# Performance work log

Hardware: AMD Instinct MI355X
Metric: run time of the kernel (lower is better)

## Reference

```python
import jax, jax.numpy as jnp
import numpy as np

N = 2708
IN_C = 1433
OUT_C = 64


def setup_inputs() -> dict:
    key = jax.random.key(0)
    k1, k2, k3, k4, k5, k6, k7 = jax.random.split(key, 7)
    X = jax.random.normal(k1, (N, IN_C), dtype=jnp.float32)
    A = jax.random.randint(k2, (N, N), 0, 2, dtype=jnp.int32)  # dense binary adjacency mask
    # Graph Fourier basis: orthonormal-ish random matrix (QR of gaussian)
    U = jnp.linalg.qr(jax.random.normal(k3, (N, N), dtype=jnp.float32))[0]
    s = 1.0 / np.sqrt(IN_C)
    W_K = jax.random.normal(k4, (OUT_C, IN_C), dtype=jnp.float32) * s
    W_Q = jax.random.normal(k5, (OUT_C, IN_C), dtype=jnp.float32) * s
    W_V = jax.random.normal(k6, (OUT_C, IN_C), dtype=jnp.float32) * s
    lmbd = jax.random.uniform(k7, (N, 1), dtype=jnp.float32)
    return {"X": X, "A": A, "U": U, "W_K": W_K, "W_Q": W_Q, "W_V": W_V, "lmbd": lmbd}


def reference(X, A, U, W_K, W_Q, W_V, lmbd):
    # Linear projections (torch nn.Linear: x @ W.T)
    K = X @ W_K.T  # [N, d]
    Q = X @ W_Q.T  # [N, d]
    V = X @ W_V.T  # [N, d]
    d_k = K.shape[-1]
    E = (Q @ K.T) / d_k  # [N, N]
    # spectral filtering: igft(lmbd * gft(E)) = U @ (lmbd * (U^T @ E))
    E = jnp.abs(U @ (lmbd * (U.T @ E)))
    # masked softmax over neighbors; dropout p=0 in eval mode (no-op)
    E_masked = jnp.where(A == 0, -jnp.inf, E)
    alpha = jax.nn.softmax(E_masked, axis=-1)
    H = alpha @ V  # [N, d]
    return H
```

## Files before the change

kernel.cpp:

```cpp
#include <hip/hip_runtime.h>

#define NV 2708
#define INC 1433
#define XCOLS 1472
#define UDIM 2752
#define PSTR 2728
#define BSTR 2752
#define SLAB ((size_t)(2752*64))
#define MWPR 88
#define NSP 4
#define NSU 11

typedef __attribute__((ext_vector_type(8))) short bf16x8;
typedef __attribute__((ext_vector_type(4))) float f32x4;
typedef __attribute__((ext_vector_type(4))) unsigned short u16x4;

__device__ __forceinline__ unsigned short f2bf(float f){
  union { float f; unsigned int i; } v; v.f = f;
  return (unsigned short)((v.i + 0x7fffu + ((v.i >> 16) & 1u)) >> 16);
}

__device__ __forceinline__ void conv_row(const float* __restrict__ src,
                                         unsigned short* __restrict__ dst, int tid){
  const int sh = ((unsigned int)((size_t)src >> 2)) & 1;
  if (tid == 0){ int ce = sh ? 0 : (INC - 1); dst[ce] = f2bf(src[ce]); }
  const float2* s2 = (const float2*)(src + sh);
  for (int c2 = tid; c2 < (INC - 1)/2; c2 += 256){
    float2 v = s2[c2];
    int c = sh + c2*2;
    dst[c]     = f2bf(v.x);
    dst[c + 1] = f2bf(v.y);
  }
  for (int c = INC + tid; c < XCOLS; c += 256) dst[c] = 0;
}

__global__ __launch_bounds__(256) void convert_all(
    const float* __restrict__ X, const float* __restrict__ WK,
    const float* __restrict__ WQ, const float* __restrict__ WV,
    const float* __restrict__ U, const int* __restrict__ A,
    unsigned short* __restrict__ Xbf, unsigned short* __restrict__ Wbf,
    unsigned short* __restrict__ Ubf, unsigned short* __restrict__ UTbf,
    unsigned int* __restrict__ Abits)
{
  __shared__ __align__(16) float tpose[64][68];
  const int bx = blockIdx.x;
  const int tid = threadIdx.x;
  if (bx < 2752){
    const int row = bx;
    unsigned short* dst = Xbf + (size_t)row*XCOLS;
    if (row < NV){
      conv_row(X + (size_t)row*INC, dst, tid);
    } else {
      u16x4 zz = {0,0,0,0};
      for (int c4 = tid; c4 < XCOLS/4; c4 += 256) *(u16x4*)(dst + c4*4) = zz;
    }
  } else if (bx < 2944){
    const int row = bx - 2752;
    const float* s = (row < 64) ? WK : (row < 128) ? WQ : WV;
    conv_row(s + (size_t)(row & 63)*INC, Wbf + (size_t)row*XCOLS, tid);
  } else if (bx < 5652){
    const int i = bx - 2944;
    const int lane = tid & 63, wave = tid >> 6;
    const int* arow = A + (size_t)i*NV;
    unsigned int* drow = Abits + (size_t)i*MWPR;
    for (int g = wave; g < 11; g += 4){
      int base = g*256 + lane*4;
      int4 v = make_int4(0,0,0,0);
      if (base < NV) v = *(const int4*)(arow + base);
      unsigned long long m0 = __ballot(v.x != 0);
      unsigned long long m1 = __ballot(v.y != 0);
      unsigned long long m2 = __ballot(v.z != 0);
      unsigned long long m3 = __ballot(v.w != 0);
      if (lane < 8){
        unsigned long long mm = (lane < 2) ? m0 : (lane < 4) ? m1 : (lane < 6) ? m2 : m3;
        drow[g*8 + lane] = (lane & 1) ? (unsigned int)(mm >> 32) : (unsigned int)mm;
      }
    }
  } else {
    const int t = bx - 5652;
    const int tx = t % 43, ty = t / 43;
    const int r0 = ty*64, c0 = tx*64;
    #pragma unroll
    for (int j = 0; j < 4; j++){
      int row = j*16 + (tid >> 4);
      int c4  = (tid & 15)*4;
      float4 v = make_float4(0.f,0.f,0.f,0.f);
      if (r0 + row < NV && c0 + c4 < NV)
        v = *(const float4*)(U + (size_t)(r0+row)*NV + c0 + c4);
      *(float4*)&tpose[row][c4] = v;
      u16x4 h = { f2bf(v.x), f2bf(v.y), f2bf(v.z), f2bf(v.w) };
      *(u16x4*)(Ubf + (size_t)(r0+row)*UDIM + c0 + c4) = h;
    }
    __syncthreads();
    const int i = tid >> 2;
    #pragma unroll
    for (int j = 0; j < 4; j++){
      int kk = ((tid & 3) + j*4)*4;
      u16x4 h = { f2bf(tpose[kk+0][i]), f2bf(tpose[kk+1][i]),
                  f2bf(tpose[kk+2][i]), f2bf(tpose[kk+3][i]) };
      *(u16x4*)(UTbf + (size_t)(c0+i)*UDIM + r0 + kk) = h;
    }
  }
}

__global__ __launch_bounds__(256) void proj(
    const unsigned short* __restrict__ Xbf, const unsigned short* __restrict__ Wbf,
    float* __restrict__ part)
{
  __shared__ __align__(16) unsigned short At[32*72];
  __shared__ __align__(16) unsigned short Bt[64*72];
  const int tid = threadIdx.x;
  const int lane = tid & 63, wave = tid >> 6, quad = lane >> 4, lr = lane & 15;
  const int m0 = blockIdx.x * 32;
  const int s  = blockIdx.y, z = blockIdx.z;
  const int kbeg = s * 384, kend = min(kbeg + 384, XCOLS);
  const int wm = (wave & 1) * 16, wn = (wave >> 1) * 32;
  const unsigned short* Wz = Wbf + (size_t)z*64*XCOLS;
  const int arow = tid >> 3, aseg = tid & 7;
  const int brow = tid >> 2, bseg = tid & 3;
  f32x4 acc[2] = {};

  for (int k0 = kbeg; k0 < kend; k0 += 64){
    *(bf16x8*)&At[arow*72 + aseg*8] =
        *(const bf16x8*)(Xbf + (size_t)(m0+arow)*XCOLS + k0 + aseg*8);
    {
      const unsigned short* b = Wz + (size_t)brow*XCOLS + k0 + bseg*16;
      *(bf16x8*)&Bt[brow*72 + bseg*16]     = *(const bf16x8*)(b);
      *(bf16x8*)&Bt[brow*72 + bseg*16 + 8] = *(const bf16x8*)(b + 8);
    }
    __syncthreads();
    #pragma unroll
    for (int ks = 0; ks < 2; ks++){
      bf16x8 af = *(const bf16x8*)&At[(wm + lr)*72 + ks*32 + quad*8];
      bf16x8 bv[2];
      #pragma unroll
      for (int t = 0; t < 2; t++)
        bv[t] = *(const bf16x8*)&Bt[(wn + t*16 + lr)*72 + ks*32 + quad*8];
      #pragma unroll
      for (int t = 0; t < 2; t++)
        acc[t] = __builtin_amdgcn_mfma_f32_16x16x32_bf16(af, bv[t], acc[t], 0, 0, 0);
    }
    __syncthreads();
  }
  float* dst = part + (size_t)(z*NSP + s) * SLAB;
  #pragma unroll
  for (int t = 0; t < 2; t++)
    #pragma unroll
    for (int e = 0; e < 4; e++)
      dst[(size_t)(m0 + wm + quad*4 + e)*64 + wn + t*16 + lr] = acc[t][e];
}

__global__ __launch_bounds__(256) void reduce_proj(
    const float* __restrict__ part, unsigned short* __restrict__ K16f,
    unsigned short* __restrict__ QT16, unsigned short* __restrict__ VTf)
{
  int idx = blockIdx.x*256 + threadIdx.x;
  int z = blockIdx.y;
  int m = idx >> 6, c = idx & 63;
  const float* base = part + (size_t)z*NSP*SLAB + idx;
  float v = 0.f;
  #pragma unroll
  for (int s = 0; s < NSP; s++) v += base[s*SLAB];
  unsigned short h = (m < NV) ? f2bf(v) : (unsigned short)0;
  if (z == 0){
    if (m < 2720) K16f[((m>>4)*2 + (c>>5))*512 + (m&15)*32 + (c&31)] = h;
  } else if (z == 1){
    QT16[(size_t)c*BSTR + m] = h;
  } else {
    if (m < 2720) VTf[(m>>5)*2048 + c*32 + (m&31)] = h;
  }
}

__global__ __launch_bounds__(256) void gemmU(
    const unsigned short* __restrict__ Arow, const unsigned short* __restrict__ Bcm,
    float* __restrict__ part)
{
  __shared__ __align__(16) unsigned short At[32*72];
  __shared__ __align__(16) unsigned short Bt[64*72];
  const int tid = threadIdx.x;
  const int lane = tid & 63, wave = tid >> 6, quad = lane >> 4, lr = lane & 15;
  const int m0 = blockIdx.x * 32;
  const int s  = blockIdx.y;
  const int kbeg = s * 256, kend = min(kbeg + 256, UDIM);
  const int wm = (wave & 1) * 16, wn = (wave >> 1) * 32;
  const int arow = tid >> 3, aseg = tid & 7;
  const int bc = tid >> 2, bseg = tid & 3;
  f32x4 acc[2] = {};

  for (int k0 = kbeg; k0 < kend; k0 += 64){
    *(bf16x8*)&At[arow*72 + aseg*8] =
        *(const bf16x8*)(Arow + (size_t)(m0+arow)*UDIM + k0 + aseg*8);
    {
      const unsigned short* b = Bcm + (size_t)bc*BSTR + k0 + bseg*16;
      *(bf16x8*)&Bt[bc*72 + bseg*16]     = *(const bf16x8*)(b);
      *(bf16x8*)&Bt[bc*72 + bseg*16 + 8] = *(const bf16x8*)(b + 8);
    }
    __syncthreads();
    #pragma unroll
    for (int ks = 0; ks < 2; ks++){
      bf16x8 af = *(const bf16x8*)&At[(wm + lr)*72 + ks*32 + quad*8];
      bf16x8 bv[2];
      #pragma unroll
      for (int t = 0; t < 2; t++)
        bv[t] = *(const bf16x8*)&Bt[(wn + t*16 + lr)*72 + ks*32 + quad*8];
      #pragma unroll
      for (int t = 0; t < 2; t++)
        acc[t] = __builtin_amdgcn_mfma_f32_16x16x32_bf16(af, bv[t], acc[t], 0, 0, 0);
    }
    __syncthreads();
  }
  float* dst = part + (size_t)s * SLAB;
  #pragma unroll
  for (int t = 0; t < 2; t++)
    #pragma unroll
    for (int e = 0; e < 4; e++)
      dst[(size_t)(m0 + wm + quad*4 + e)*64 + wn + t*16 + lr] = acc[t][e];
}

__global__ __launch_bounds__(256) void reduce_g(
    const float* __restrict__ part, const float* __restrict__ lm,
    unsigned short* __restrict__ G2T)
{
  int idx = blockIdx.x*256 + threadIdx.x;
  int m = idx >> 6, c = idx & 63;
  const float* base = part + idx;
  float v = 0.f;
  #pragma unroll
  for (int s = 0; s < NSU; s++) v += base[s*SLAB];
  unsigned short h = 0;
  if (m < NV) h = f2bf(v * lm[m] * (1.0f/64.0f));
  G2T[(size_t)c*BSTR + m] = h;
}

__global__ __launch_bounds__(512) void fused_attn(
    const float* __restrict__ partF, const unsigned short* __restrict__ K16f,
    const unsigned int* __restrict__ Abits, const unsigned short* __restrict__ VTf,
    float* __restrict__ Hout)
{
  __shared__ __align__(16) unsigned short pbuf[16*PSTR];
  __shared__ __align__(16) unsigned short fbuf[16*64];
  __shared__ unsigned int mrow[16*MWPR];
  __shared__ float swave[8][16];
  __shared__ float rinv[16];
  __shared__ __align__(16) float obuf[4][256];
  const int tid  = threadIdx.x;
  const int lane = tid & 63, wave = tid >> 6;
  const int quad = lane >> 4, lr = lane & 15;
  const int i0 = blockIdx.x * 16;

  #pragma unroll
  for (int h = 0; h < 2; h++){
    int idx = h*512 + tid;
    const float* base = partF + (size_t)(i0 + (idx >> 6))*64 + (idx & 63);
    float v = 0.f;
    #pragma unroll
    for (int s = 0; s < NSU; s++) v += base[s*SLAB];
    fbuf[idx] = f2bf(v);
  }
  for (int idx = tid; idx < 16*MWPR; idx += 512){
    int r = idx / MWPR;
    unsigned int v = 0;
    if (i0 + r < NV) v = Abits[(size_t)(i0 + r)*MWPR + (idx - r*MWPR)];
    mrow[idx] = v;
  }
  __syncthreads();

  const bf16x8 af0 = *(const bf16x8*)&fbuf[lr*64 + quad*8];
  const bf16x8 af1 = *(const bf16x8*)&fbuf[lr*64 + 32 + quad*8];
  float psum[4] = {0.f, 0.f, 0.f, 0.f};
  {
    int t = wave;
    const unsigned short* kb = K16f + t*1024 + lr*32 + quad*8;
    bf16x8 b0 = *(const bf16x8*)(kb);
    bf16x8 b1 = *(const bf16x8*)(kb + 512);
    while (t < 170){
      int tn = t + 8;
      bf16x8 n0 = b0, n1 = b1;
      if (tn < 170){
        const unsigned short* nb = K16f + tn*1024 + lr*32 + quad*8;
        n0 = *(const bf16x8*)(nb);
        n1 = *(const bf16x8*)(nb + 512);
      }
      f32x4 sv0 = {}, sv1 = {};
      sv0 = __builtin_amdgcn_mfma_f32_16x16x32_bf16(af0, b0, sv0, 0, 0, 0);
      sv1 = __builtin_amdgcn_mfma_f32_16x16x32_bf16(af1, b1, sv1, 0, 0, 0);
      f32x4 sv = sv0 + sv1;
      {
        int col = t*16 + lr;
        int ss = col & 255, ll = ss >> 2;
        int wsh = (col >> 8)*8 + (ss & 3)*2 + (ll >> 5);
        int bit = ll & 31;
        #pragma unroll
        for (int e = 0; e < 4; e++){
          int r = quad*4 + e;
          float p = 0.f;
          if ((mrow[r*MWPR + wsh] >> bit) & 1u) p = __expf(fabsf(sv[e]));
          psum[e] += p;
          pbuf[r*PSTR + col] = f2bf(p);
        }
      }
      b0 = n0; b1 = n1; t = tn;
    }
  }
  #pragma unroll
  for (int e = 0; e < 4; e++){
    float v = psum[e];
    #pragma unroll
    for (int o = 1; o <= 8; o <<= 1) v += __shfl_xor(v, o, 64);
    if (lr == 0) swave[wave][quad*4 + e] = v;
  }
  __syncthreads();
  if (tid < 16){
    float s = 0.f;
    #pragma unroll
    for (int w = 0; w < 8; w++) s += swave[w][tid];
    rinv[tid] = (s > 0.f) ? (1.f/s) : 0.f;
  }
  __syncthreads();

  const int c0 = (wave & 3) * 16;
  const int ktbeg = (wave >> 2) ? 43 : 0;
  const int ktend = (wave >> 2) ? 85 : 43;
  f32x4 acc = {};
  {
    bf16x8 bv = *(const bf16x8*)&VTf[ktbeg*2048 + (c0 + lr)*32 + quad*8];
    for (int kt = ktbeg; kt < ktend; kt++){
      bf16x8 bn = bv;
      if (kt + 1 < ktend) bn = *(const bf16x8*)&VTf[(kt+1)*2048 + (c0 + lr)*32 + quad*8];
      bf16x8 af = *(const bf16x8*)&pbuf[lr*PSTR + kt*32 + quad*8];
      acc = __builtin_amdgcn_mfma_f32_16x16x32_bf16(af, bv, acc, 0, 0, 0);
      bv = bn;
    }
  }
  if (wave >= 4) *(f32x4*)&obuf[wave & 3][lane*4] = acc;
  __syncthreads();
  if (wave < 4){
    f32x4 o = *(const f32x4*)&obuf[wave][lane*4];
    acc += o;
    #pragma unroll
    for (int e = 0; e < 4; e++){
      int r = quad*4 + e;
      int i = i0 + r;
      if (i < NV) Hout[(size_t)i*64 + c0 + lr] = acc[e] * rinv[r];
    }
  }
}

extern "C" void kernel_launch(void* const* d_in, const int* in_sizes, int n_in,
                              void* d_out, int out_size, void* d_ws, size_t ws_size,
                              hipStream_t stream){
  (void)in_sizes; (void)n_in; (void)out_size; (void)ws_size;
  const float* X  = (const float*)d_in[0];
  const int*   A  = (const int*)d_in[1];
  const float* U  = (const float*)d_in[2];
  const float* WK = (const float*)d_in[3];
  const float* WQ = (const float*)d_in[4];
  const float* WV = (const float*)d_in[5];
  const float* lm = (const float*)d_in[6];

  char* ws = (char*)d_ws;
  size_t off = 0;
  auto alloc = [&](size_t bytes){ size_t o = off; off = (off + bytes + 255) & ~(size_t)255; return o; };
  float*          part = (float*)(ws + alloc(12*SLAB*4));
  unsigned short* Ubf  = (unsigned short*)(ws + alloc((size_t)UDIM*UDIM*2));
  unsigned short* UTbf = (unsigned short*)(ws + alloc((size_t)UDIM*UDIM*2));
  unsigned short* Xbf  = (unsigned short*)(ws + alloc((size_t)UDIM*XCOLS*2));
  unsigned short* Wbf  = (unsigned short*)(ws + alloc((size_t)192*XCOLS*2));
  unsigned short* K16f = (unsigned short*)(ws + alloc((size_t)170*1024*2));
  unsigned short* QT16 = (unsigned short*)(ws + alloc((size_t)64*BSTR*2));
  unsigned short* G2T  = (unsigned short*)(ws + alloc((size_t)64*BSTR*2));
  unsigned short* VTf  = (unsigned short*)(ws + alloc((size_t)85*2048*2));
  unsigned int*   Abits= (unsigned int*)(ws + alloc((size_t)NV*MWPR*4));

  convert_all<<<dim3(7501), 256, 0, stream>>>(X, WK, WQ, WV, U, A,
                                              Xbf, Wbf, Ubf, UTbf, Abits);
  proj<<<dim3(86, NSP, 3), 256, 0, stream>>>(Xbf, Wbf, part);
  reduce_proj<<<dim3(688, 3), 256, 0, stream>>>(part, K16f, QT16, VTf);
  gemmU<<<dim3(86, NSU), 256, 0, stream>>>(UTbf, QT16, part);
  reduce_g<<<dim3(688), 256, 0, stream>>>(part, lm, G2T);
  gemmU<<<dim3(86, NSU), 256, 0, stream>>>(Ubf, G2T, part);
  fused_attn<<<dim3(170), 512, 0, stream>>>(part, K16f, Abits, VTf, (float*)d_out);
}
```

Before: 176.5 us.

## Overlap U conversion and adjacency bit-packing with projection GEMM blocks

Moves the U bf16 conversion/transposition and the adjacency bitmask packing out of the convert kernel and into extra blocks of the projection kernel, so this memory-bound work runs alongside the projection MFMA blocks. The Q projection is no longer split along K: a single block per row tile computes the full reduction and writes the transposed bf16 QT directly, which removes Q from the partial-sum buffer and from the reduce pass. The intent is to cut serial dependency and shorten the convert kernel. In exchange, the projection grid gets much larger, with many early-exit blocks, and Q now runs as a long serial K loop across only a few blocks.

After: 179.9 us. Within noise of the previous version (+1.9%).

```diff
diff --git a/kernel.cpp b/kernel.cpp
--- a/kernel.cpp
+++ b/kernel.cpp
@@ -37,12 +37,8 @@
 __global__ __launch_bounds__(256) void convert_all(
     const float* __restrict__ X, const float* __restrict__ WK,
     const float* __restrict__ WQ, const float* __restrict__ WV,
-    const float* __restrict__ U, const int* __restrict__ A,
-    unsigned short* __restrict__ Xbf, unsigned short* __restrict__ Wbf,
-    unsigned short* __restrict__ Ubf, unsigned short* __restrict__ UTbf,
-    unsigned int* __restrict__ Abits)
-{
-  __shared__ __align__(16) float tpose[64][68];
+    unsigned short* __restrict__ Xbf, unsigned short* __restrict__ Wbf)
+{
   const int bx = blockIdx.x;
   const int tid = threadIdx.x;
   if (bx < 2752){
@@ -54,66 +50,86 @@
       u16x4 zz = {0,0,0,0};
       for (int c4 = tid; c4 < XCOLS/4; c4 += 256) *(u16x4*)(dst + c4*4) = zz;
     }
-  } else if (bx < 2944){
+  } else {
     const int row = bx - 2752;
     const float* s = (row < 64) ? WK : (row < 128) ? WQ : WV;
     conv_row(s + (size_t)(row & 63)*INC, Wbf + (size_t)row*XCOLS, tid);
-  } else if (bx < 5652){
-    const int i = bx - 2944;
-    const int lane = tid & 63, wave = tid >> 6;
-    const int* arow = A + (size_t)i*NV;
-    unsigned int* drow = Abits + (size_t)i*MWPR;
-    for (int g = wave; g < 11; g += 4){
-      int base = g*256 + lane*4;
-      int4 v = make_int4(0,0,0,0);
-      if (base < NV) v = *(const int4*)(arow + base);
-      unsigned long long m0 = __ballot(v.x != 0);
-      unsigned long long m1 = __ballot(v.y != 0);
-      unsigned long long m2 = __ballot(v.z != 0);
-      unsigned long long m3 = __ballot(v.w != 0);
-      if (lane < 8){
-        unsigned long long mm = (lane < 2) ? m0 : (lane < 4) ? m1 : (lane < 6) ? m2 : m3;
-        drow[g*8 + lane] = (lane & 1) ? (unsigned int)(mm >> 32) : (unsigned int)mm;
-      }
-    }
-  } else {
-    const int t = bx - 5652;
-    const int tx = t % 43, ty = t / 43;
-    const int r0 = ty*64, c0 = tx*64;
-    #pragma unroll
-    for (int j = 0; j < 4; j++){
-      int row = j*16 + (tid >> 4);
-      int c4  = (tid & 15)*4;
-      float4 v = make_float4(0.f,0.f,0.f,0.f);
-      if (r0 + row < NV && c0 + c4 < NV)
-        v = *(const float4*)(U + (size_t)(r0+row)*NV + c0 + c4);
-      *(float4*)&tpose[row][c4] = v;
-      u16x4 h = { f2bf(v.x), f2bf(v.y), f2bf(v.z), f2bf(v.w) };
-      *(u16x4*)(Ubf + (size_t)(r0+row)*UDIM + c0 + c4) = h;
-    }
-    __syncthreads();
-    const int i = tid >> 2;
-    #pragma unroll
-    for (int j = 0; j < 4; j++){
-      int kk = ((tid & 3) + j*4)*4;
-      u16x4 h = { f2bf(tpose[kk+0][i]), f2bf(tpose[kk+1][i]),
-                  f2bf(tpose[kk+2][i]), f2bf(tpose[kk+3][i]) };
-      *(u16x4*)(UTbf + (size_t)(c0+i)*UDIM + r0 + kk) = h;
-    }
   }
 }
 
 __global__ __launch_bounds__(256) void proj(
     const unsigned short* __restrict__ Xbf, const unsigned short* __restrict__ Wbf,
-    float* __restrict__ part)
-{
-  __shared__ __align__(16) unsigned short At[32*72];
-  __shared__ __align__(16) unsigned short Bt[64*72];
+    const float* __restrict__ U, const int* __restrict__ A,
+    float* __restrict__ part, unsigned short* __restrict__ QT16,
+    unsigned short* __restrict__ Ubf, unsigned short* __restrict__ UTbf,
+    unsigned int* __restrict__ Abits)
+{
+  __shared__ __align__(16) char smem[17408];
   const int tid = threadIdx.x;
+  const int bx = blockIdx.x;
+  const int s = blockIdx.y, z = blockIdx.z;
+
+  if (bx >= 86){
+    const int slot = s*3 + z;
+    if (bx < 312){
+      const int i = (bx - 86)*12 + slot;
+      if (i < NV){
+        const int lane = tid & 63, wave = tid >> 6;
+        const int* arow = A + (size_t)i*NV;
+        unsigned int* drow = Abits + (size_t)i*MWPR;
+        for (int g = wave; g < 11; g += 4){
+          int base = g*256 + lane*4;
+          int4 v = make_int4(0,0,0,0);
+          if (base < NV) v = *(const int4*)(arow + base);
+          unsigned long long m0 = __ballot(v.x != 0);
+          unsigned long long m1 = __ballot(v.y != 0);
+          unsigned long long m2 = __ballot(v.z != 0);
+          unsigned long long m3 = __ballot(v.w != 0);
+          if (lane < 8){
+            unsigned long long mm = (lane < 2) ? m0 : (lane < 4) ? m1 : (lane < 6) ? m2 : m3;
+            drow[g*8 + lane] = (lane & 1) ? (unsigned int)(mm >> 32) : (unsigned int)mm;
+          }
+        }
+      }
+    } else {
+      const int t = (bx - 312)*12 + slot;
+      if (t < 1849){
+        float* tpose = (float*)smem;
+        const int tx = t % 43, ty = t / 43;
+        const int r0 = ty*64, c0 = tx*64;
+        #pragma unroll
+        for (int j = 0; j < 4; j++){
+          int row = j*16 + (tid >> 4);
+          int c4  = (tid & 15)*4;
+          float4 v = make_float4(0.f,0.f,0.f,0.f);
+          if (r0 + row < NV && c0 + c4 < NV)
+            v = *(const float4*)(U + (size_t)(r0+row)*NV + c0 + c4);
+          *(float4*)&tpose[row*68 + c4] = v;
+          u16x4 h = { f2bf(v.x), f2bf(v.y), f2bf(v.z), f2bf(v.w) };
+          *(u16x4*)(Ubf + (size_t)(r0+row)*UDIM + c0 + c4) = h;
+        }
+        __syncthreads();
+        const int i = tid >> 2;
+        #pragma unroll
+        for (int j = 0; j < 4; j++){
+          int kk = ((tid & 3) + j*4)*4;
+          u16x4 h = { f2bf(tpose[(kk+0)*68 + i]), f2bf(tpose[(kk+1)*68 + i]),
+                      f2bf(tpose[(kk+2)*68 + i]), f2bf(tpose[(kk+3)*68 + i]) };
+          *(u16x4*)(UTbf + (size_t)(c0+i)*UDIM + r0 + kk) = h;
+        }
+      }
+    }
+    return;
+  }
+
+  const bool isQ = (z == 1);
+  if (isQ && s) return;
+  unsigned short* At = (unsigned short*)smem;
+  unsigned short* Bt = (unsigned short*)(smem + 4608);
   const int lane = tid & 63, wave = tid >> 6, quad = lane >> 4, lr = lane & 15;
-  const int m0 = blockIdx.x * 32;
-  const int s  = blockIdx.y, z = blockIdx.z;
-  const int kbeg = s * 384, kend = min(kbeg + 384, XCOLS);
+  const int m0 = bx * 32;
+  const int kbeg = isQ ? 0 : s * 384;
+  const int kend = isQ ? XCOLS : min(kbeg + 384, XCOLS);
   const int wm = (wave & 1) * 16, wn = (wave >> 1) * 32;
   const unsigned short* Wz = Wbf + (size_t)z*64*XCOLS;
   const int arow = tid >> 3, aseg = tid & 7;
@@ -142,32 +158,40 @@
     }
     __syncthreads();
   }
-  float* dst = part + (size_t)(z*NSP + s) * SLAB;
-  #pragma unroll
-  for (int t = 0; t < 2; t++)
-    #pragma unroll
-    for (int e = 0; e < 4; e++)
-      dst[(size_t)(m0 + wm + quad*4 + e)*64 + wn + t*16 + lr] = acc[t][e];
+  if (isQ){
+    #pragma unroll
+    for (int t = 0; t < 2; t++)
+      #pragma unroll
+      for (int e = 0; e < 4; e++){
+        int m = m0 + wm + quad*4 + e;
+        int c = wn + t*16 + lr;
+        QT16[(size_t)c*BSTR + m] = f2bf(acc[t][e]);
+      }
+  } else {
+    float* dst = part + (size_t)((z == 2 ? NSP : 0) + s) * SLAB;
+    #pragma unroll
+    for (int t = 0; t < 2; t++)
+      #pragma unroll
+      for (int e = 0; e < 4; e++)
+        dst[(size_t)(m0 + wm + quad*4 + e)*64 + wn + t*16 + lr] = acc[t][e];
+  }
 }
 
 __global__ __launch_bounds__(256) void reduce_proj(
     const float* __restrict__ part, unsigned short* __restrict__ K16f,
-    unsigned short* __restrict__ QT16, unsigned short* __restrict__ VTf)
+    unsigned short* __restrict__ VTf)
 {
   int idx = blockIdx.x*256 + threadIdx.x;
-  int z = blockIdx.y;
+  int zv = blockIdx.y;
   int m = idx >> 6, c = idx & 63;
-  const float* base = part + (size_t)z*NSP*SLAB + idx;
+  const float* base = part + (size_t)(zv ? NSP : 0)*SLAB + idx;
   float v = 0.f;
   #pragma unroll
   for (int s = 0; s < NSP; s++) v += base[s*SLAB];
-  unsigned short h = (m < NV) ? f2bf(v) : (unsigned short)0;
-  if (z == 0){
-    if (m < 2720) K16f[((m>>4)*2 + (c>>5))*512 + (m&15)*32 + (c&31)] = h;
-  } else if (z == 1){
-    QT16[(size_t)c*BSTR + m] = h;
-  } else {
-    if (m < 2720) VTf[(m>>5)*2048 + c*32 + (m&31)] = h;
+  if (m < 2720){
+    unsigned short h = (m < NV) ? f2bf(v) : (unsigned short)0;
+    if (zv == 0) K16f[((m>>4)*2 + (c>>5))*512 + (m&15)*32 + (c&31)] = h;
+    else         VTf[(m>>5)*2048 + c*32 + (m&31)] = h;
   }
 }
 
@@ -361,7 +385,7 @@
   char* ws = (char*)d_ws;
   size_t off = 0;
   auto alloc = [&](size_t bytes){ size_t o = off; off = (off + bytes + 255) & ~(size_t)255; return o; };
-  float*          part = (float*)(ws + alloc(12*SLAB*4));
+  float*          part = (float*)(ws + alloc(11*SLAB*4));
   unsigned short* Ubf  = (unsigned short*)(ws + alloc((size_t)UDIM*UDIM*2));
   unsigned short* UTbf = (unsigned short*)(ws + alloc((size_t)UDIM*UDIM*2));
   unsigned short* Xbf  = (unsigned short*)(ws + alloc((size_t)UDIM*XCOLS*2));
@@ -372,10 +396,10 @@
   unsigned short* VTf  = (unsigned short*)(ws + alloc((size_t)85*2048*2));
   unsigned int*   Abits= (unsigned int*)(ws + alloc((size_t)NV*MWPR*4));
 
-  convert_all<<<dim3(7501), 256, 0, stream>>>(X, WK, WQ, WV, U, A,
-                                              Xbf, Wbf, Ubf, UTbf, Abits);
-  proj<<<dim3(86, NSP, 3), 256, 0, stream>>>(Xbf, Wbf, part);
-  reduce_proj<<<dim3(688, 3), 256, 0, stream>>>(part, K16f, QT16, VTf);
+  convert_all<<<dim3(2944), 256, 0, stream>>>(X, WK, WQ, WV, Xbf, Wbf);
+  proj<<<dim3(467, NSP, 3), 256, 0, stream>>>(Xbf, Wbf, U, A, part, QT16,
+                                              Ubf, UTbf, Abits);
+  reduce_proj<<<dim3(688, 2), 256, 0, stream>>>(part, K16f, VTf);
   gemmU<<<dim3(86, NSU), 256, 0, stream>>>(UTbf, QT16, part);
   reduce_g<<<dim3(688), 256, 0, stream>>>(part, lm, G2T);
   gemmU<<<dim3(86, NSU), 256, 0, stream>>>(Ubf, G2T, part);
```

## Fuse second U GEMM into attention kernel, computing per-block F rows via MFMA

Applied to the files above, without the earlier changes.

Drops the separate gemmU launch that computed U @ G2 into split-K partial slabs. fused_attn now computes its own 16 rows of F directly from Ubf and G2T with bf16 MFMA, splitting K across 8 waves and reducing through shared memory. This removes a kernel launch and the 11-way partial-sum read traffic. In exchange, only 170 blocks perform the full K=2752 reduction serially, with no split-K parallelism across the GPU.

After: 176.7 us. No clear change (+0.1%).

```diff
diff --git a/kernel.cpp b/kernel.cpp
--- a/kernel.cpp
+++ b/kernel.cpp
@@ -233,7 +233,8 @@
 }
 
 __global__ __launch_bounds__(512) void fused_attn(
-    const float* __restrict__ partF, const unsigned short* __restrict__ K16f,
+    const unsigned short* __restrict__ Ubf, const unsigned short* __restrict__ G2T,
+    const unsigned short* __restrict__ K16f,
     const unsigned int* __restrict__ Abits, const unsigned short* __restrict__ VTf,
     float* __restrict__ Hout)
 {
@@ -248,20 +249,37 @@
   const int quad = lane >> 4, lr = lane & 15;
   const int i0 = blockIdx.x * 16;
 
-  #pragma unroll
-  for (int h = 0; h < 2; h++){
-    int idx = h*512 + tid;
-    const float* base = partF + (size_t)(i0 + (idx >> 6))*64 + (idx & 63);
-    float v = 0.f;
-    #pragma unroll
-    for (int s = 0; s < NSU; s++) v += base[s*SLAB];
-    fbuf[idx] = f2bf(v);
+  float* fpart = (float*)pbuf;
+  {
+    f32x4 facc[4] = {};
+    const unsigned short* ua = Ubf + (size_t)(i0 + lr)*UDIM + quad*8;
+    for (int ks = wave; ks < 86; ks += 8){
+      const int k0 = ks*32;
+      bf16x8 af = *(const bf16x8*)(ua + k0);
+      #pragma unroll
+      for (int n = 0; n < 4; n++){
+        bf16x8 bv = *(const bf16x8*)(G2T + (size_t)(n*16 + lr)*BSTR + k0 + quad*8);
+        facc[n] = __builtin_amdgcn_mfma_f32_16x16x32_bf16(af, bv, facc[n], 0, 0, 0);
+      }
+    }
+    #pragma unroll
+    for (int n = 0; n < 4; n++)
+      *(f32x4*)&fpart[(wave*4 + n)*256 + lane*4] = facc[n];
   }
   for (int idx = tid; idx < 16*MWPR; idx += 512){
     int r = idx / MWPR;
     unsigned int v = 0;
     if (i0 + r < NV) v = Abits[(size_t)(i0 + r)*MWPR + (idx - r*MWPR)];
     mrow[idx] = v;
+  }
+  __syncthreads();
+  for (int idx = tid; idx < 1024; idx += 512){
+    int n = idx >> 8, l4 = idx & 255;
+    float v = 0.f;
+    #pragma unroll
+    for (int w = 0; w < 8; w++) v += fpart[(w*4 + n)*256 + l4];
+    int l = l4 >> 2, e = l4 & 3;
+    fbuf[((l >> 4)*4 + e)*64 + n*16 + (l & 15)] = f2bf(v);
   }
   __syncthreads();
 
@@ -378,6 +396,5 @@
   reduce_proj<<<dim3(688, 3), 256, 0, stream>>>(part, K16f, QT16, VTf);
   gemmU<<<dim3(86, NSU), 256, 0, stream>>>(UTbf, QT16, part);
   reduce_g<<<dim3(688), 256, 0, stream>>>(part, lm, G2T);
-  gemmU<<<dim3(86, NSU), 256, 0, stream>>>(Ubf, G2T, part);
-  fused_attn<<<dim3(170), 512, 0, stream>>>(part, K16f, Abits, VTf, (float*)d_out);
-}
+  fused_attn<<<dim3(170), 512, 0, stream>>>(Ubf, G2T, K16f, Abits, VTf, (float*)d_out);
+}
```
